# Optimization experiments

Hardware: AMD Instinct MI355X
Metric: run time of the kernel (lower is better)

The kernel has to match this reference:

```python
import jax, jax.numpy as jnp
import numpy as np

CH = 512
NUM_GROUPS = 32
EPS = 1e-6

def _xavier(key, shape):
    fan_in, fan_out = shape[1], shape[0]
    limit = np.sqrt(6.0 / (fan_in + fan_out))
    return jax.random.uniform(key, shape, jnp.float32, -limit, limit)

def setup_inputs() -> dict:
    key = jax.random.key(0)
    ks = jax.random.split(key, 6)
    B, C, H, W = 32, CH, 32, 32
    x = jax.random.normal(ks[0], (B, C, H, W), jnp.float32)
    # 1x1 conv weights stored as [C_out, C_in]; biases zero (per initialize())
    wq = _xavier(ks[1], (C, C)); wk = _xavier(ks[2], (C, C))
    wv = _xavier(ks[3], (C, C)); wp = _xavier(ks[4], (C, C))
    bq = jnp.zeros((C,)); bk = jnp.zeros((C,)); bv = jnp.zeros((C,)); bp = jnp.zeros((C,))
    gn_w = jnp.ones((C,)); gn_b = jnp.zeros((C,))
    return {"x": x, "gn_w": gn_w, "gn_b": gn_b,
            "wq": wq, "bq": bq, "wk": wk, "bk": bk,
            "wv": wv, "bv": bv, "wp": wp, "bp": bp}

def _group_norm(x, w, b):
    B, C, H, W = x.shape
    g = NUM_GROUPS
    xg = x.reshape(B, g, C // g, H, W)
    mean = xg.mean(axis=(2, 3, 4), keepdims=True)
    var = xg.var(axis=(2, 3, 4), keepdims=True)
    xn = ((xg - mean) * jax.lax.rsqrt(var + EPS)).reshape(B, C, H, W)
    return xn * w[None, :, None, None] + b[None, :, None, None]

def reference(x, gn_w, gn_b, wq, bq, wk, bk, wv, bv, wp, bp):
    B, C, H, W = x.shape
    h = _group_norm(x, gn_w, gn_b)
    hf = h.reshape(B, C, H * W)  # [B, C, N]
    # 1x1 convs == per-pixel linear over channels
    q = jnp.einsum('oc,bcn->bno', wq, hf) + bq  # [B, N, C]
    k = jnp.einsum('oc,bcn->bon', wk, hf) + bk[None, :, None]  # [B, C, N]
    v = jnp.einsum('oc,bcn->bno', wv, hf) + bv  # [B, N, C]
    attn = jnp.einsum('bqc,bck->bqk', q, k) * (C ** -0.5)  # [B, N, N]
    attn = jax.nn.softmax(attn, axis=-1)
    out = jnp.einsum('bqk,bkc->bqc', attn, v)  # [B, N, C]
    out = jnp.einsum('oc,bnc->bon', wp, out) + bp[None, :, None]  # [B, C, N]
    return x + out.reshape(B, C, H, W)
```

## Files before the change

kernel.cpp:

```cpp
#include <hip/hip_runtime.h>


#define C_DIM 512
#define N_PIX 1024
#define BATCH 32
#define CPG 16
#define EPS 1e-6f
#define SCALE 0.044194173824159216f
#define ESTRIDE 66
#define ESTRU   72
#define ES2     40

typedef unsigned short u16;
typedef __attribute__((ext_vector_type(8))) short bf16x8;
typedef __attribute__((ext_vector_type(4))) float f32x4;
typedef __attribute__((ext_vector_type(2))) float f32x2;

static __device__ __forceinline__ float bf2f(u16 u) {
    union { unsigned int i; float f; } v; v.i = ((unsigned int)u) << 16; return v.f;
}
static __device__ __forceinline__ u16 f2bf(float f) {
    union { float f; unsigned int i; } v; v.f = f;
    unsigned int r = v.i + 0x7fffu + ((v.i >> 16) & 1u);
    return (u16)(r >> 16);
}

static __device__ __forceinline__ void gl_lds16(const u16* g, u16* l) {
    __builtin_amdgcn_global_load_lds(
        (const __attribute__((address_space(1))) unsigned int*)g,
        (__attribute__((address_space(3))) unsigned int*)l,
        16, 0, 0);
}

#define BAR()   __builtin_amdgcn_s_barrier()
#define SCHED() __builtin_amdgcn_sched_barrier(0x7)

__global__ __launch_bounds__(256) void prep_kernel(
        const float* __restrict__ wq, const float* __restrict__ wk,
        const float* __restrict__ wv, const float* __restrict__ wp,
        u16* __restrict__ out, const float* __restrict__ x,
        float* __restrict__ stats) {
    int blk = blockIdx.x;
    if (blk < 1024) {
        int i = blk * 256 + threadIdx.x;
        int mat = i >> 16;
        const float* src = (mat == 0) ? wq : (mat == 1) ? wk : (mat == 2) ? wv : wp;
        float4 v = ((const float4*)src)[i & 65535];
        ushort4 o;
        o.x = f2bf(v.x); o.y = f2bf(v.y); o.z = f2bf(v.z); o.w = f2bf(v.w);
        *(ushort4*)&out[(size_t)i * 4] = o;
        return;
    }
    blk -= 1024;
    int b = blk >> 5, g = blk & 31;
    const float4* xv = (const float4*)(x + ((size_t)(b * C_DIM + g * CPG)) * N_PIX);
    int tid = threadIdx.x;
    float s = 0.f, sq = 0.f;
#pragma unroll 4
    for (int i = tid; i < (CPG * N_PIX) / 4; i += 256) {
        float4 v = xv[i];
        s  += v.x + v.y + v.z + v.w;
        sq += v.x * v.x + v.y * v.y + v.z * v.z + v.w * v.w;
    }
#pragma unroll
    for (int m = 1; m < 64; m <<= 1) {
        s += __shfl_xor(s, m);
        sq += __shfl_xor(sq, m);
    }
    __shared__ float rs[4], rq[4];
    int wv_ = tid >> 6;
    if ((tid & 63) == 0) { rs[wv_] = s; rq[wv_] = sq; }
    __syncthreads();
    if (tid == 0) {
        float S = rs[0] + rs[1] + rs[2] + rs[3];
        float Q = rq[0] + rq[1] + rq[2] + rq[3];
        float mean = S * (1.0f / (CPG * N_PIX));
        float var  = Q * (1.0f / (CPG * N_PIX)) - mean * mean;
        stats[blk * 2] = mean;
        stats[blk * 2 + 1] = rsqrtf(var + EPS);
    }
}

__global__ __launch_bounds__(256) void gnt_kernel(
        const float* __restrict__ x, const float* __restrict__ gw,
        const float* __restrict__ gb, const float* __restrict__ stats,
        u16* __restrict__ h) {
    int blk = blockIdx.x;
    int b = blk >> 4, nc = blk & 15;
    int n0 = nc * 64;
    __shared__ u16 T[64 * 520];
    int tid = threadIdx.x;
    int cq = tid >> 4;
    int n4 = tid & 15;
    const float* xb = x + (size_t)b * C_DIM * N_PIX + n0;
#pragma unroll 4
    for (int pass = 0; pass < 32; ++pass) {
        int c = pass * 16 + cq;
        int g = c >> 4;
        float mean = stats[(b * 32 + g) * 2];
        float inv  = stats[(b * 32 + g) * 2 + 1];
        float sc = gw[c] * inv;
        float sh = gb[c] - mean * sc;
        float4 v = *(const float4*)(xb + (size_t)c * N_PIX + n4 * 4);
        int nn = n4 * 4;
        T[(nn + 0) * 520 + c] = f2bf(v.x * sc + sh);
        T[(nn + 1) * 520 + c] = f2bf(v.y * sc + sh);
        T[(nn + 2) * 520 + c] = f2bf(v.z * sc + sh);
        T[(nn + 3) * 520 + c] = f2bf(v.w * sc + sh);
    }
    __syncthreads();
    u16* hb = h + ((size_t)b * N_PIX + n0) * C_DIM;
    int rr = tid >> 5;
    int cc = (tid & 31) * 16;
#pragma unroll
    for (int p = 0; p < 8; ++p) {
        int n = p * 8 + rr;
        bf16x8 v0 = *(const bf16x8*)&T[n * 520 + cc];
        bf16x8 v1 = *(const bf16x8*)&T[n * 520 + cc + 8];
        *(bf16x8*)&hb[(size_t)n * C_DIM + cc] = v0;
        *(bf16x8*)&hb[(size_t)n * C_DIM + cc + 8] = v1;
    }
}


#define MM32(mq) do { \
    _Pragma("unroll") \
    for (int t_ = 0; t_ < 4; ++t_) { \
        _Pragma("unroll") \
        for (int n_ = 0; n_ < 2; ++n_) \
            acc[(mq)*4 + t_][n_] = \
                __builtin_amdgcn_mfma_f32_16x16x32_bf16( \
                    af[t_], bf[n_], acc[(mq)*4 + t_][n_], 0, 0, 0); \
    } \
} while (0)

template <int MODE>
__global__ __launch_bounds__(512, 4) void gemm32_kernel(
        const u16* __restrict__ A, const u16* __restrict__ B,
        void* __restrict__ Cv, void* __restrict__ Cv2,
        const float* __restrict__ bias, const float* __restrict__ bias2,
        int K, int rsA, int rsB, int rsC,
        long long bsA, long long bsB, long long bsC) {
    int flat = blockIdx.x;
    int t = (flat & 7) * 128 + (flat >> 3);

    const u16 *gA, *gB;
    void* out;
    const float* bi_p;
    int cb, colb, rowb;
    if (MODE == 0) {
        int bx = t & 3, by = (t >> 2) & 3, z = t >> 4;
        int mat = z & 1, b = z >> 1;
        gA = A + (size_t)b * bsA + (size_t)by * 256 * rsA;
        gB = B + (size_t)mat * 262144 + (size_t)bx * 128 * rsB;
        out = mat ? Cv2 : Cv;
        bi_p = mat ? bias2 : bias;
        cb = b; colb = bx * 128; rowb = by * 256;
    } else {
        int bx = t & 7, by = (t >> 3) & 3, b = t >> 5;
        gA = A + (size_t)b * bsA + (size_t)by * 256 * rsA;
        gB = B + (size_t)b * bsB + (size_t)bx * 128 * rsB;
        out = (b >= 16) ? Cv2 : Cv;
        bi_p = nullptr;
        cb = b & 15; colb = bx * 128; rowb = by * 256;
    }

    __shared__ __align__(16) u16 smem[24576];

    int tid = threadIdx.x;
    int lane = tid & 63, wave = tid >> 6;
    int wm = wave >> 2, wn = wave & 3;
    int quad = lane >> 4, l15 = lane & 15;
    int srow = tid >> 2;
    int lg = (tid & 3) ^ ((srow >> 1) & 3);

    const int nk = K >> 5;
    const int nit = nk >> 1;

    auto STGA = [&](int buf, int hh, int kt) {
        const u16* src = gA + (size_t)(hh * 128 + srow) * rsA + (size_t)kt * 32 + lg * 8;
        u16* dst = &smem[buf * 12288 + (hh * 128 + srow) * 32 + (tid & 3) * 8];
        gl_lds16(src, dst);
    };
    auto STGB = [&](int buf, int kt) {
        const u16* src = gB + (size_t)srow * rsB + (size_t)kt * 32 + lg * 8;
        u16* dst = &smem[buf * 12288 + 8192 + srow * 32 + (tid & 3) * 8];
        gl_lds16(src, dst);
    };
    auto LDA32 = [&](int buf, int mq, int t_) -> bf16x8 {
        int r = wm * 128 + mq * 64 + t_ * 16 + l15;
        return *(const bf16x8*)&smem[buf * 12288 + r * 32 +
                                     ((quad ^ ((r >> 1) & 3)) << 3)];
    };
    auto LDB32 = [&](int buf, int nt) -> bf16x8 {
        int r = wn * 32 + nt * 16 + l15;
        return *(const bf16x8*)&smem[buf * 12288 + 8192 + r * 32 +
                                     ((quad ^ ((r >> 1) & 3)) << 3)];
    };

    f32x4 acc[8][2];
#pragma unroll
    for (int mt = 0; mt < 8; ++mt)
#pragma unroll
        for (int nt = 0; nt < 2; ++nt)
            acc[mt][nt] = (f32x4){0.f, 0.f, 0.f, 0.f};
    bf16x8 af[4], bf[2];

    STGA(0, 0, 0); STGA(0, 1, 0); STGB(0, 0); STGB(1, 1);
    asm volatile("s_waitcnt vmcnt(1)" ::: "memory");
    SCHED(); BAR(); SCHED();

    for (int it = 0; it < nit; ++it) {
        const bool s = (it + 1 < nit);
        const int k1 = 2 * it + 1, k2 = 2 * it + 2, k3 = 2 * it + 3;

#pragma unroll
        for (int t_ = 0; t_ < 4; ++t_) af[t_] = LDA32(0, 0, t_);
#pragma unroll
        for (int n = 0; n < 2; ++n) bf[n] = LDB32(0, n);
        STGA(1, 0, k1); STGA(1, 1, k1);
        SCHED(); BAR(); SCHED();
        __builtin_amdgcn_s_setprio(1); MM32(0); __builtin_amdgcn_s_setprio(0);
        SCHED(); BAR(); SCHED();

#pragma unroll
        for (int t_ = 0; t_ < 4; ++t_) af[t_] = LDA32(0, 1, t_);
        if (s) STGB(0, k2);
        SCHED(); BAR(); SCHED();
        __builtin_amdgcn_s_setprio(1); MM32(1); __builtin_amdgcn_s_setprio(0);
        if (s) asm volatile("s_waitcnt vmcnt(1)" ::: "memory");
        else   asm volatile("s_waitcnt vmcnt(0)" ::: "memory");
        SCHED(); BAR(); SCHED();

#pragma unroll
        for (int t_ = 0; t_ < 4; ++t_) af[t_] = LDA32(1, 0, t_);
#pragma unroll
        for (int n = 0; n < 2; ++n) bf[n] = LDB32(1, n);
        if (s) { STGA(0, 0, k2); STGA(0, 1, k2); }
        SCHED(); BAR(); SCHED();
        __builtin_amdgcn_s_setprio(1); MM32(0); __builtin_amdgcn_s_setprio(0);
        SCHED(); BAR(); SCHED();

#pragma unroll
        for (int t_ = 0; t_ < 4; ++t_) af[t_] = LDA32(1, 1, t_);
        if (s) STGB(1, k3);
        SCHED(); BAR(); SCHED();
        __builtin_amdgcn_s_setprio(1); MM32(1); __builtin_amdgcn_s_setprio(0);
        if (s) asm volatile("s_waitcnt vmcnt(1)" ::: "memory");
        SCHED(); BAR(); SCHED();
    }

    int colb_w = colb + wn * 32;
    int rowb_w = rowb + wm * 128;
    u16* ebw = smem + wave * (16 * ES2);
    int lr = lane >> 2;
    int ec = (lane & 3) * 8;
    float bcol[2];
    if (MODE == 0) {
#pragma unroll
        for (int nt = 0; nt < 2; ++nt)
            bcol[nt] = bi_p[colb_w + nt * 16 + l15];
    }
#pragma unroll
    for (int mt = 0; mt < 8; ++mt) {
#pragma unroll
        for (int nt = 0; nt < 2; ++nt) {
            f32x4 a = acc[mt][nt];
#pragma unroll
            for (int reg = 0; reg < 4; ++reg) {
                float fv = a[reg];
                if (MODE == 0) fv += bcol[nt];
                else fv *= SCALE;
                ebw[(quad * 4 + reg) * ES2 + nt * 16 + l15] = f2bf(fv);
            }
        }
        bf16x8 vv = *(const bf16x8*)&ebw[lr * ES2 + ec];
        size_t cidx = (size_t)cb * bsC + (size_t)(rowb_w + mt * 16 + lr) * rsC
                      + colb_w + ec;
        *(bf16x8*)&((u16*)out)[cidx] = vv;
    }
}


#define MM(mq, nq) do { \
    _Pragma("unroll") \
    for (int t_ = 0; t_ < 4; ++t_) { \
        _Pragma("unroll") \
        for (int n_ = 0; n_ < 2; ++n_) { \
            _Pragma("unroll") \
            for (int ks_ = 0; ks_ < 2; ++ks_) \
                acc[(mq)*4 + t_][(nq)*2 + n_] = \
                    __builtin_amdgcn_mfma_f32_16x16x32_bf16( \
                        af[t_][ks_], bf[(nq)*2 + n_][ks_], \
                        acc[(mq)*4 + t_][(nq)*2 + n_], 0, 0, 0); \
        } \
    } \
} while (0)

template <int MODE>
__global__ __launch_bounds__(512, 2) void gemm_kernel(
        const u16* __restrict__ A, const u16* __restrict__ A2,
        const u16* __restrict__ B, const u16* __restrict__ B2,
        void* __restrict__ Cv, void* __restrict__ Cv2,
        const float* __restrict__ bias, const float* __restrict__ xres,
        int K, int rsA, int rsB, int rsC,
        long long bsA, long long bsB, long long bsC,
        int nx, int ny) {
    int flat = blockIdx.x;
    int t = (flat & 7) * 32 + (flat >> 3);
    int bx = t % nx, by = (t / nx) % ny, bz = t / (nx * ny);
    int b = bz;
    const u16 *gA, *gB;
    void* out = Cv;
    if (MODE == 3) {
        gA = ((b >= 16) ? A2 : A) + (size_t)(b & 15) * bsA + (size_t)by * 256 * rsA;
        gB = B + (size_t)b * bsB + (size_t)bx * 256 * rsB;
        out = (b >= 16) ? Cv2 : Cv;
    } else if (MODE == 4) {
        gA = A + (size_t)by * 256 * rsA;
        gB = ((b >= 16) ? B2 : B) + (size_t)(b & 15) * bsB + (size_t)bx * 256 * rsB;
    } else {
        gA = A + (size_t)by * 256 * rsA;
        gB = B + (size_t)b * bsB + (size_t)bx * 256 * rsB;
    }
    int cb = (MODE == 3) ? (b & 15) : b;

    __shared__ __align__(16) u16 smem[65536];

    int tid = threadIdx.x;
    int lane = tid & 63, wave = tid >> 6;
    int wm = wave >> 2, wn = wave & 3;
    int quad = lane >> 4, l15 = lane & 15, l7 = lane & 7;
    int srow = tid >> 3;
    int lg = (tid & 7) ^ (srow & 7);

    const int nk = K >> 6;
    const int nit = nk >> 1;

    auto STG = [&](const u16* g, int rs, int buf, int isB, int hh, int kt) {
        const u16* src = g + (size_t)(hh * 128 + srow) * rs + (size_t)kt * 64 + lg * 8;
        u16* dst = &smem[buf * 32768 + isB * 16384 + (hh * 128 + srow) * 64 + (tid & 7) * 8];
        gl_lds16(src, dst);
        gl_lds16(src + (size_t)64 * rs, dst + 4096);
    };
    auto LDA = [&](int buf, int mq, int t_, int ks) -> bf16x8 {
        return *(const bf16x8*)&smem[buf * 32768 +
            (wm * 128 + mq * 64 + t_ * 16 + l15) * 64 + (((ks * 4 + quad) ^ l7) << 3)];
    };
    auto LDB = [&](int buf, int nt, int ks) -> bf16x8 {
        return *(const bf16x8*)&smem[buf * 32768 + 16384 +
            (wn * 64 + nt * 16 + l15) * 64 + (((ks * 4 + quad) ^ l7) << 3)];
    };

    f32x4 acc[8][4];
#pragma unroll
    for (int mt = 0; mt < 8; ++mt)
#pragma unroll
        for (int nt = 0; nt < 4; ++nt)
            acc[mt][nt] = (f32x4){0.f, 0.f, 0.f, 0.f};
    bf16x8 af[4][2], bf[4][2];

    STG(gB, rsB, 0, 1, 0, 0); STG(gB, rsB, 0, 1, 1, 0);
    STG(gA, rsA, 0, 0, 0, 0); STG(gA, rsA, 0, 0, 1, 0);
    STG(gB, rsB, 1, 1, 0, 1); STG(gB, rsB, 1, 1, 1, 1);
    asm volatile("s_waitcnt vmcnt(4)" ::: "memory");
    SCHED(); BAR(); SCHED();

    for (int it = 0; it < nit; ++it) {
        const bool s = (it + 1 < nit);
        const int k1 = 2 * it + 1, k2 = 2 * it + 2, k3 = 2 * it + 3;

#pragma unroll
        for (int t_ = 0; t_ < 4; ++t_)
#pragma unroll
            for (int ks = 0; ks < 2; ++ks) af[t_][ks] = LDA(0, 0, t_, ks);
#pragma unroll
        for (int n = 0; n < 2; ++n)
#pragma unroll
            for (int ks = 0; ks < 2; ++ks) bf[n][ks] = LDB(0, n, ks);
        STG(gA, rsA, 1, 0, 0, k1);
        SCHED(); BAR(); SCHED();
        __builtin_amdgcn_s_setprio(1); MM(0, 0); __builtin_amdgcn_s_setprio(0);
        SCHED(); BAR(); SCHED();

#pragma unroll
        for (int n = 2; n < 4; ++n)
#pragma unroll
            for (int ks = 0; ks < 2; ++ks) bf[n][ks] = LDB(0, n, ks);
        STG(gA, rsA, 1, 0, 1, k1);
        SCHED(); BAR(); SCHED();
        __builtin_amdgcn_s_setprio(1); MM(0, 1); __builtin_amdgcn_s_setprio(0);
        SCHED(); BAR(); SCHED();

#pragma unroll
        for (int t_ = 0; t_ < 4; ++t_)
#pragma unroll
            for (int ks = 0; ks < 2; ++ks) af[t_][ks] = LDA(0, 1, t_, ks);
        if (s) STG(gB, rsB, 0, 1, 0, k2);
        SCHED(); BAR(); SCHED();
        __builtin_amdgcn_s_setprio(1); MM(1, 1); __builtin_amdgcn_s_setprio(0);
        SCHED(); BAR(); SCHED();

        if (s) STG(gB, rsB, 0, 1, 1, k2);
        SCHED(); BAR(); SCHED();
        __builtin_amdgcn_s_setprio(1); MM(1, 0); __builtin_amdgcn_s_setprio(0);
        if (s) asm volatile("s_waitcnt vmcnt(4)" ::: "memory");
        else   asm volatile("s_waitcnt vmcnt(0)" ::: "memory");
        SCHED(); BAR(); SCHED();

#pragma unroll
        for (int t_ = 0; t_ < 4; ++t_)
#pragma unroll
            for (int ks = 0; ks < 2; ++ks) af[t_][ks] = LDA(1, 0, t_, ks);
#pragma unroll
        for (int n = 0; n < 2; ++n)
#pragma unroll
            for (int ks = 0; ks < 2; ++ks) bf[n][ks] = LDB(1, n, ks);
        if (s) STG(gA, rsA, 0, 0, 0, k2);
        SCHED(); BAR(); SCHED();
        __builtin_amdgcn_s_setprio(1); MM(0, 0); __builtin_amdgcn_s_setprio(0);
        SCHED(); BAR(); SCHED();

#pragma unroll
        for (int n = 2; n < 4; ++n)
#pragma unroll
            for (int ks = 0; ks < 2; ++ks) bf[n][ks] = LDB(1, n, ks);
        if (s) STG(gA, rsA, 0, 0, 1, k2);
        SCHED(); BAR(); SCHED();
        __builtin_amdgcn_s_setprio(1); MM(0, 1); __builtin_amdgcn_s_setprio(0);
        SCHED(); BAR(); SCHED();

#pragma unroll
        for (int t_ = 0; t_ < 4; ++t_)
#pragma unroll
            for (int ks = 0; ks < 2; ++ks) af[t_][ks] = LDA(1, 1, t_, ks);
        if (s) STG(gB, rsB, 1, 1, 0, k3);
        SCHED(); BAR(); SCHED();
        __builtin_amdgcn_s_setprio(1); MM(1, 1); __builtin_amdgcn_s_setprio(0);
        SCHED(); BAR(); SCHED();

        if (s) STG(gB, rsB, 1, 1, 1, k3);
        SCHED(); BAR(); SCHED();
        __builtin_amdgcn_s_setprio(1); MM(1, 0); __builtin_amdgcn_s_setprio(0);
        if (s) asm volatile("s_waitcnt vmcnt(4)" ::: "memory");
        SCHED(); BAR(); SCHED();
    }

    int colb = bx * 256 + wn * 64;
    int rowb = by * 256 + wm * 128;

    if (MODE == 4) {
        float* ebw = (float*)(smem + 32768) + wave * (16 * ESTRIDE);
        int er = lane >> 4;
        int ec4 = (lane & 15) * 4;
#pragma unroll
        for (int mt = 0; mt < 8; ++mt) {
#pragma unroll
            for (int nt = 0; nt < 4; ++nt) {
                f32x4 a = acc[mt][nt];
#pragma unroll
                for (int reg = 0; reg < 4; ++reg)
                    ebw[(quad * 4 + reg) * ESTRIDE + nt * 16 + l15] = a[reg];
            }
#pragma unroll
            for (int j = 0; j < 4; ++j) {
                int lr = er + 4 * j;
                f32x2 v0 = *(f32x2*)&ebw[lr * ESTRIDE + ec4];
                f32x2 v1 = *(f32x2*)&ebw[lr * ESTRIDE + ec4 + 2];
                int gr = rowb + mt * 16 + lr;
                int gc = colb + ec4;
                size_t cidx = (size_t)cb * bsC + (size_t)gr * rsC + gc;
                float bi = bias[gr];
                float4 xr = *(const float4*)&xres[cidx];
                float4 st = make_float4(v0.x + bi + xr.x, v0.y + bi + xr.y,
                                        v1.x + bi + xr.z, v1.y + bi + xr.w);
                *(float4*)&((float*)out)[cidx] = st;
            }
        }
    } else {
        u16* ebw = (smem + 32768) + wave * (16 * ESTRU);
        int er = lane >> 3;
        int ec = (lane & 7) * 8;
#pragma unroll
        for (int mt = 0; mt < 8; ++mt) {
            float4 brow = make_float4(0.f, 0.f, 0.f, 0.f);
            if (MODE == 1)
                brow = *(const float4*)&bias[rowb + mt * 16 + quad * 4];
#pragma unroll
            for (int nt = 0; nt < 4; ++nt) {
                f32x4 a = acc[mt][nt];
#pragma unroll
                for (int reg = 0; reg < 4; ++reg) {
                    float fv = a[reg];
                    if (MODE == 1) fv += ((const float*)&brow)[reg];
                    ebw[(quad * 4 + reg) * ESTRU + nt * 16 + l15] = f2bf(fv);
                }
            }
#pragma unroll
            for (int j = 0; j < 2; ++j) {
                int lr = er + 8 * j;
                bf16x8 vv = *(const bf16x8*)&ebw[lr * ESTRU + ec];
                int gr = rowb + mt * 16 + lr;
                size_t cidx = (size_t)cb * bsC + (size_t)gr * rsC + colb + ec;
                *(bf16x8*)&((u16*)out)[cidx] = vv;
            }
        }
    }
}

__global__ __launch_bounds__(256) void softmax_kernel(
        u16* __restrict__ S0, u16* __restrict__ S1) {
    int row = blockIdx.x * 4 + (threadIdx.x >> 6);
    int lane = threadIdx.x & 63;
    u16* p = ((row & 16384) ? S1 : S0) + (size_t)(row & 16383) * N_PIX + lane * 16;
    bf16x8 u0 = *(const bf16x8*)p;
    bf16x8 u1 = *(const bf16x8*)(p + 8);
    float f[16];
#pragma unroll
    for (int i = 0; i < 8; ++i) {
        f[i] = bf2f((u16)u0[i]);
        f[8 + i] = bf2f((u16)u1[i]);
    }
    float m = f[0];
#pragma unroll
    for (int i = 1; i < 16; ++i) m = fmaxf(m, f[i]);
#pragma unroll
    for (int off = 1; off < 64; off <<= 1) m = fmaxf(m, __shfl_xor(m, off));
    float s = 0.f;
#pragma unroll
    for (int i = 0; i < 16; ++i) { f[i] = __expf(f[i] - m); s += f[i]; }
#pragma unroll
    for (int off = 1; off < 64; off <<= 1) s += __shfl_xor(s, off);
    float inv = 1.0f / s;
    bf16x8 s0, s1;
#pragma unroll
    for (int i = 0; i < 8; ++i) {
        s0[i] = (short)f2bf(f[i] * inv);
        s1[i] = (short)f2bf(f[8 + i] * inv);
    }
    *(bf16x8*)p = s0;
    *(bf16x8*)(p + 8) = s1;
}

extern "C" void kernel_launch(void* const* d_in, const int* in_sizes, int n_in,
                              void* d_out, int out_size, void* d_ws, size_t ws_size,
                              hipStream_t stream) {
    const float* x    = (const float*)d_in[0];
    const float* gn_w = (const float*)d_in[1];
    const float* gn_b = (const float*)d_in[2];
    const float* wq   = (const float*)d_in[3];
    const float* bq   = (const float*)d_in[4];
    const float* wk   = (const float*)d_in[5];
    const float* bk   = (const float*)d_in[6];
    const float* wv   = (const float*)d_in[7];
    const float* bv   = (const float*)d_in[8];
    const float* wp   = (const float*)d_in[9];
    const float* bp   = (const float*)d_in[10];
    float* y = (float*)d_out;

    const size_t BCN = (size_t)BATCH * C_DIM * N_PIX;
    char* w = (char*)d_ws;
    u16* h  = (u16*)(w);
    u16* q  = (u16*)(w + 2 * BCN);
    u16* k  = (u16*)(w + 4 * BCN);
    u16* v  = (u16*)(w + 6 * BCN);
    u16* Or = (u16*)(w + 8 * BCN);
    u16* wb = (u16*)(w + 10 * BCN);
    u16* wvb = wb + 524288, *wpb = wb + 786432;
    float* stats = (float*)(w + 10 * BCN + 2 * 1024 * 1024);
    u16* S0 = h;
    u16* S1 = Or;
    u16* O0 = q;
    u16* O1 = k;

    const long long BS = 524288;
    const long long SB = 1048576;

    prep_kernel<<<2048, 256, 0, stream>>>(wq, wk, wv, wp, wb, x, stats);
    gnt_kernel<<<512, 256, 0, stream>>>(x, gn_w, gn_b, stats, h);

    gemm32_kernel<0><<<1024, 512, 0, stream>>>(
        h, wb, q, k, bq, bk, 512, 512, 512, 512, BS, 0, BS);
    gemm_kernel<1><<<256, 512, 0, stream>>>(
        wvb, nullptr, h, nullptr, v, nullptr, bv, nullptr,
        512, 512, 512, 1024, 0, BS, BS, 4, 2);

    gemm32_kernel<2><<<1024, 512, 0, stream>>>(
        q, k, S0, S1, nullptr, nullptr, 512, 512, 512, 1024, BS, BS, SB);
    softmax_kernel<<<8192, 256, 0, stream>>>(S0, S1);
    gemm_kernel<3><<<256, 512, 0, stream>>>(
        S0, S1, v, nullptr, O0, O1, nullptr, nullptr,
        1024, 1024, 1024, 512, SB, BS, BS, 2, 4);

    gemm_kernel<4><<<256, 512, 0, stream>>>(
        wpb, nullptr, O0, O1, y, nullptr, bp, x,
        512, 512, 512, 1024, 0, BS, BS, 4, 2);
}
```

Before: 337.6 us.

## Fuse group-norm statistics and normalize-transpose into one LDS-resident kernel

Group-norm statistics and the normalize/transpose to pixel-major bf16 now happen in one kernel per (batch, group). Each block stages its 16x1024 slice of x in padded shared memory, computes mean and variance, then writes 32-byte packed bf16 rows. This drops the second global read of x and the stats round trip, and splits weight conversion into its own kernel. In exchange it uses about 64KB of LDS per block, which limits occupancy, and the output writes are 32-byte chunks strided by rows.

```diff
diff --git a/kernel.cpp b/kernel.cpp
--- a/kernel.cpp
+++ b/kernel.cpp
@@ -10,6 +10,7 @@
 #define ESTRIDE 66
 #define ESTRU   72
 #define ES2     40
+#define GPAD    1028
 
 typedef unsigned short u16;
 typedef __attribute__((ext_vector_type(8))) short bf16x8;
@@ -35,90 +36,76 @@
 #define BAR()   __builtin_amdgcn_s_barrier()
 #define SCHED() __builtin_amdgcn_sched_barrier(0x7)
 
-__global__ __launch_bounds__(256) void prep_kernel(
+__global__ __launch_bounds__(256) void wconv_kernel(
         const float* __restrict__ wq, const float* __restrict__ wk,
         const float* __restrict__ wv, const float* __restrict__ wp,
-        u16* __restrict__ out, const float* __restrict__ x,
-        float* __restrict__ stats) {
+        u16* __restrict__ out) {
+    int i = blockIdx.x * 256 + threadIdx.x;
+    int mat = i >> 16;
+    const float* src = (mat == 0) ? wq : (mat == 1) ? wk : (mat == 2) ? wv : wp;
+    float4 v = ((const float4*)src)[i & 65535];
+    ushort4 o;
+    o.x = f2bf(v.x); o.y = f2bf(v.y); o.z = f2bf(v.z); o.w = f2bf(v.w);
+    *(ushort4*)&out[(size_t)i * 4] = o;
+}
+
+__global__ __launch_bounds__(256) void gn_kernel(
+        const float* __restrict__ x, const float* __restrict__ gw,
+        const float* __restrict__ gb, u16* __restrict__ h) {
     int blk = blockIdx.x;
-    if (blk < 1024) {
-        int i = blk * 256 + threadIdx.x;
-        int mat = i >> 16;
-        const float* src = (mat == 0) ? wq : (mat == 1) ? wk : (mat == 2) ? wv : wp;
-        float4 v = ((const float4*)src)[i & 65535];
-        ushort4 o;
-        o.x = f2bf(v.x); o.y = f2bf(v.y); o.z = f2bf(v.z); o.w = f2bf(v.w);
-        *(ushort4*)&out[(size_t)i * 4] = o;
-        return;
-    }
-    blk -= 1024;
     int b = blk >> 5, g = blk & 31;
+    __shared__ float xl[16 * GPAD + 16];
+    int tid = threadIdx.x;
     const float4* xv = (const float4*)(x + ((size_t)(b * C_DIM + g * CPG)) * N_PIX);
-    int tid = threadIdx.x;
+
     float s = 0.f, sq = 0.f;
-#pragma unroll 4
-    for (int i = tid; i < (CPG * N_PIX) / 4; i += 256) {
+#pragma unroll
+    for (int p = 0; p < 16; ++p) {
+        int i = p * 256 + tid;
         float4 v = xv[i];
         s  += v.x + v.y + v.z + v.w;
         sq += v.x * v.x + v.y * v.y + v.z * v.z + v.w * v.w;
+        *(float4*)&xl[(i >> 8) * GPAD + (i & 255) * 4] = v;
     }
 #pragma unroll
     for (int m = 1; m < 64; m <<= 1) {
         s += __shfl_xor(s, m);
         sq += __shfl_xor(sq, m);
     }
-    __shared__ float rs[4], rq[4];
     int wv_ = tid >> 6;
-    if ((tid & 63) == 0) { rs[wv_] = s; rq[wv_] = sq; }
+    if ((tid & 63) == 0) {
+        xl[16 * GPAD + wv_] = s;
+        xl[16 * GPAD + 4 + wv_] = sq;
+    }
     __syncthreads();
-    if (tid == 0) {
-        float S = rs[0] + rs[1] + rs[2] + rs[3];
-        float Q = rq[0] + rq[1] + rq[2] + rq[3];
-        float mean = S * (1.0f / (CPG * N_PIX));
-        float var  = Q * (1.0f / (CPG * N_PIX)) - mean * mean;
-        stats[blk * 2] = mean;
-        stats[blk * 2 + 1] = rsqrtf(var + EPS);
-    }
-}
-
-__global__ __launch_bounds__(256) void gnt_kernel(
-        const float* __restrict__ x, const float* __restrict__ gw,
-        const float* __restrict__ gb, const float* __restrict__ stats,
-        u16* __restrict__ h) {
-    int blk = blockIdx.x;
-    int b = blk >> 4, nc = blk & 15;
-    int n0 = nc * 64;
-    __shared__ u16 T[64 * 520];
-    int tid = threadIdx.x;
-    int cq = tid >> 4;
-    int n4 = tid & 15;
-    const float* xb = x + (size_t)b * C_DIM * N_PIX + n0;
-#pragma unroll 4
-    for (int pass = 0; pass < 32; ++pass) {
-        int c = pass * 16 + cq;
-        int g = c >> 4;
-        float mean = stats[(b * 32 + g) * 2];
-        float inv  = stats[(b * 32 + g) * 2 + 1];
-        float sc = gw[c] * inv;
-        float sh = gb[c] - mean * sc;
-        float4 v = *(const float4*)(xb + (size_t)c * N_PIX + n4 * 4);
-        int nn = n4 * 4;
-        T[(nn + 0) * 520 + c] = f2bf(v.x * sc + sh);
-        T[(nn + 1) * 520 + c] = f2bf(v.y * sc + sh);
-        T[(nn + 2) * 520 + c] = f2bf(v.z * sc + sh);
-        T[(nn + 3) * 520 + c] = f2bf(v.w * sc + sh);
-    }
-    __syncthreads();
-    u16* hb = h + ((size_t)b * N_PIX + n0) * C_DIM;
-    int rr = tid >> 5;
-    int cc = (tid & 31) * 16;
-#pragma unroll
-    for (int p = 0; p < 8; ++p) {
-        int n = p * 8 + rr;
-        bf16x8 v0 = *(const bf16x8*)&T[n * 520 + cc];
-        bf16x8 v1 = *(const bf16x8*)&T[n * 520 + cc + 8];
-        *(bf16x8*)&hb[(size_t)n * C_DIM + cc] = v0;
-        *(bf16x8*)&hb[(size_t)n * C_DIM + cc + 8] = v1;
+    float S = xl[16 * GPAD] + xl[16 * GPAD + 1] + xl[16 * GPAD + 2] + xl[16 * GPAD + 3];
+    float Q = xl[16 * GPAD + 4] + xl[16 * GPAD + 5] + xl[16 * GPAD + 6] + xl[16 * GPAD + 7];
+    float mean = S * (1.0f / (CPG * N_PIX));
+    float var  = Q * (1.0f / (CPG * N_PIX)) - mean * mean;
+    float inv  = rsqrtf(var + EPS);
+
+    float sc[16], sh[16];
+#pragma unroll
+    for (int c = 0; c < 16; ++c) {
+        float w_ = gw[g * CPG + c];
+        sc[c] = w_ * inv;
+        sh[c] = gb[g * CPG + c] - mean * sc[c];
+    }
+
+    u16* hb = h + ((size_t)b * N_PIX) * C_DIM + g * CPG;
+#pragma unroll
+    for (int p = 0; p < 4; ++p) {
+        int n = p * 256 + tid;
+        unsigned int pk[8];
+#pragma unroll
+        for (int j = 0; j < 8; ++j) {
+            float lo = xl[(2 * j) * GPAD + n] * sc[2 * j] + sh[2 * j];
+            float hi = xl[(2 * j + 1) * GPAD + n] * sc[2 * j + 1] + sh[2 * j + 1];
+            pk[j] = (unsigned int)f2bf(lo) | ((unsigned int)f2bf(hi) << 16);
+        }
+        uint4* dst = (uint4*)(hb + (size_t)n * C_DIM);
+        dst[0] = make_uint4(pk[0], pk[1], pk[2], pk[3]);
+        dst[1] = make_uint4(pk[4], pk[5], pk[6], pk[7]);
     }
 }
 
@@ -567,7 +554,6 @@
     u16* Or = (u16*)(w + 8 * BCN);
     u16* wb = (u16*)(w + 10 * BCN);
     u16* wvb = wb + 524288, *wpb = wb + 786432;
-    float* stats = (float*)(w + 10 * BCN + 2 * 1024 * 1024);
     u16* S0 = h;
     u16* S1 = Or;
     u16* O0 = q;
@@ -576,8 +562,8 @@
     const long long BS = 524288;
     const long long SB = 1048576;
 
-    prep_kernel<<<2048, 256, 0, stream>>>(wq, wk, wv, wp, wb, x, stats);
-    gnt_kernel<<<512, 256, 0, stream>>>(x, gn_w, gn_b, stats, h);
+    wconv_kernel<<<1024, 256, 0, stream>>>(wq, wk, wv, wp, wb);
+    gn_kernel<<<1024, 256, 0, stream>>>(x, gn_w, gn_b, h);
 
     gemm32_kernel<0><<<1024, 512, 0, stream>>>(
         h, wb, q, k, bq, bk, 512, 512, 512, 512, BS, 0, BS);
```

New measurement: 345.0 us. 1.02x slower.
